# Optimization experiments

Hardware: AMD Instinct MI355X
Metric: run time of the kernel (lower is better)

The kernel has to match this reference:

```python
import jax, jax.numpy as jnp
import numpy as np

NEG_SLOPE = 0.2


def setup_inputs() -> dict:
    key = jax.random.key(0)
    k1, k2, k3, k4, k5 = jax.random.split(key, 5)
    N, E = 50000, 800000
    IN, H, O = 128, 4, 32
    x = jax.random.normal(k1, (N, IN), dtype=jnp.float32)
    edge_index = jax.random.randint(k2, (2, E), 0, N, dtype=jnp.int64)
    weight = jax.random.normal(k3, (IN, H, O), dtype=jnp.float32) * 0.05
    att_weight = jax.random.normal(k4, (H, 2 * O), dtype=jnp.float32) * 0.05
    bias = jax.random.normal(k5, (H * O,), dtype=jnp.float32) * 0.05
    return {"x": x, "edge_index": edge_index, "weight": weight,
            "att_weight": att_weight, "bias": bias}


def reference(x, edge_index, weight, att_weight, bias):
    # GAT forward, eval mode (dropout=0), concat=True.
    N = x.shape[0]
    H, O = weight.shape[1], weight.shape[2]
    # Linear transform: [N, H, O]
    h = jnp.einsum('ni,iho->nho', x, weight)
    src, dst = edge_index[0], edge_index[1]  # message src -> dst
    h_i = h[dst]   # target features per edge  [E, H, O]
    h_j = h[src]   # source features per edge  [E, H, O]
    # Attention logits: leaky_relu(att . [h_i || h_j])  -> [E, H]
    a_i, a_j = att_weight[:, :O], att_weight[:, O:]
    alpha = jnp.einsum('eho,ho->eh', h_i, a_i) + jnp.einsum('eho,ho->eh', h_j, a_j)
    alpha = jax.nn.leaky_relu(alpha, NEG_SLOPE)
    # Segment softmax over incoming edges of each dst node.
    amax = jax.ops.segment_max(alpha, dst, num_segments=N)      # [N, H]
    ex = jnp.exp(alpha - amax[dst])                             # [E, H]
    denom = jax.ops.segment_sum(ex, dst, num_segments=N)        # [N, H]
    coef = ex / (denom[dst] + 1e-16)                            # [E, H]
    # Weighted scatter-aggregate of source messages.
    out = jax.ops.segment_sum(h_j * coef[..., None], dst, num_segments=N)  # [N, H, O]
    out = out.reshape(N, H * O) + bias
    return out
```

## Files before the change

### kernel.cpp

```cpp
#include <hip/hip_runtime.h>
#include <hip/hip_fp16.h>
#include <math.h>

#define NEG_SLOPE 0.2f

typedef __attribute__((ext_vector_type(8))) short bf16x8;
typedef __attribute__((ext_vector_type(4))) short short4v;
typedef __attribute__((ext_vector_type(4))) float f32x4;
typedef __attribute__((ext_vector_type(8))) unsigned short u16x8;

__device__ __forceinline__ float lrelu(float x) { return x > 0.f ? x : NEG_SLOPE * x; }

__device__ __forceinline__ short f2bf(float f) {
    unsigned u = __float_as_uint(f);
    u += 0x7fff + ((u >> 16) & 1);
    return (short)(u >> 16);
}

__global__ __launch_bounds__(256) void k_gemm(const float* __restrict__ x,
                                              const float* __restrict__ w,
                                              const float* __restrict__ att,
                                              __half* __restrict__ hout,
                                              float* __restrict__ adi,
                                              float* __restrict__ adj,
                                              int* __restrict__ gcur, int N) {
    __shared__ short SH[24576];
    const int t = threadIdx.x;
    const int row0 = blockIdx.x * 64;

    if (blockIdx.x == 0) {
        gcur[t] = 0; gcur[t + 256] = 0; gcur[t + 512] = 0; gcur[t + 768] = 0;
    }

    #pragma unroll
    for (int i = 0; i < 8; ++i) {
        int idx = t + 256 * i;
        int r = idx >> 5, c4 = (idx & 31) * 4;
        float4 v = make_float4(0.f, 0.f, 0.f, 0.f);
        if (row0 + r < N) v = *(const float4*)(x + (size_t)(row0 + r) * 128 + c4);
        short4v sv;
        sv.x = f2bf(v.x); sv.y = f2bf(v.y); sv.z = f2bf(v.z); sv.w = f2bf(v.w);
        *(short4v*)&SH[(r * 128 + c4) ^ ((r & 7) << 3)] = sv;
    }
    {
        int c = t & 127, kh = (t >> 7) * 64;
        for (int kb = 0; kb < 16; ++kb) {
            int k = kh + kb * 4;
            short4v sv;
            sv.x = f2bf(w[(size_t)(k + 0) * 128 + c]);
            sv.y = f2bf(w[(size_t)(k + 1) * 128 + c]);
            sv.z = f2bf(w[(size_t)(k + 2) * 128 + c]);
            sv.w = f2bf(w[(size_t)(k + 3) * 128 + c]);
            *(short4v*)&SH[8192 + ((c * 128 + k) ^ ((c & 7) << 3))] = sv;
        }
    }
    __syncthreads();

    const int wv = t >> 6, lane = t & 63;
    const int lr = lane & 15, kg = lane >> 4;

    f32x4 acc[8];
    #pragma unroll
    for (int n = 0; n < 8; ++n) acc[n] = (f32x4){0.f, 0.f, 0.f, 0.f};

    #pragma unroll
    for (int kk = 0; kk < 4; ++kk) {
        const int k0 = kk * 32 + kg * 8;
        int r = wv * 16 + lr;
        bf16x8 a = *(const bf16x8*)&SH[(r * 128 + k0) ^ ((r & 7) << 3)];
        bf16x8 b[8];
        #pragma unroll
        for (int n = 0; n < 8; ++n) {
            int c = n * 16 + lr;
            b[n] = *(const bf16x8*)&SH[8192 + ((c * 128 + k0) ^ ((c & 7) << 3))];
        }
        #pragma unroll
        for (int n = 0; n < 8; ++n)
            acc[n] = __builtin_amdgcn_mfma_f32_16x16x32_bf16(a, b[n], acc[n], 0, 0, 0);
    }

    #pragma unroll
    for (int reg = 0; reg < 4; ++reg) {
        int r = row0 + wv * 16 + kg * 4 + reg;
        if (r < N) {
            __half* hp = hout + (size_t)r * 128 + lr;
            #pragma unroll
            for (int n = 0; n < 8; ++n)
                hp[n * 16] = __float2half(acc[n][reg]);
        }
    }

    __syncthreads();
    float* attF = (float*)&SH[8192];
    attF[t] = att[t];
    #pragma unroll
    for (int reg = 0; reg < 4; ++reg) {
        int row = wv * 16 + kg * 4 + reg;
        #pragma unroll
        for (int n = 0; n < 8; ++n) {
            int col = n * 16 + lr;
            SH[(row * 128 + col) ^ ((row & 7) << 3)] =
                (short)__half_as_ushort(__float2half(acc[n][reg]));
        }
    }
    __syncthreads();
    {
        int row = t >> 2, head = t & 3;
        int grow = row0 + row;
        if (grow < N) {
            float si = 0.f, sj = 0.f;
            #pragma unroll
            for (int j = 0; j < 32; ++j) {
                int jj = (j + row) & 31;
                float hv = __half2float(__ushort_as_half(
                    (unsigned short)SH[(row * 128 + head * 32 + jj) ^ ((row & 7) << 3)]));
                si += hv * attF[head * 64 + jj];
                sj += hv * attF[head * 64 + 32 + jj];
            }
            adi[grow * 4 + head] = si;
            adj[grow * 4 + head] = sj;
        }
    }
}

__global__ __launch_bounds__(512) void k_bin(const int* __restrict__ ei,
                                             int* __restrict__ gcur,
                                             unsigned* __restrict__ bins,
                                             int E, int nbkt, int cap) {
    __shared__ int lcnt[1024];
    __shared__ int lbase[1024];
    const int t = threadIdx.x;
    lcnt[t] = 0; lcnt[t + 512] = 0;
    __syncthreads();

    const int e0 = blockIdx.x * 4096;
    const int ne = min(4096, E - e0);

    int bkt[8], rank[8];
    unsigned pk[8];
    #pragma unroll
    for (int k = 0; k < 8; ++k) {
        int idx = t + k * 512;
        if (idx < ne) {
            int e = e0 + idx;
            int src = ei[e], dst = ei[E + e];
            int b = dst >> 6;
            bkt[k] = b;
            pk[k] = ((unsigned)(dst & 63) << 24) | (unsigned)src;
            rank[k] = atomicAdd(&lcnt[b], 1);
        } else bkt[k] = -1;
    }
    __syncthreads();
    for (int j = t; j < nbkt; j += 512)
        if (lcnt[j] > 0) lbase[j] = atomicAdd(&gcur[j], lcnt[j]);
    __syncthreads();
    #pragma unroll
    for (int k = 0; k < 8; ++k) {
        if (bkt[k] >= 0)
            bins[(size_t)bkt[k] * cap + lbase[bkt[k]] + rank[k]] = pk[k];
    }
}

#define CSR_MAX 1536

__global__ __launch_bounds__(512) void k_bucket_node(
        const unsigned* __restrict__ bins,
        const int* __restrict__ gcur,
        const __half* __restrict__ h,
        const float* __restrict__ adi,
        const float* __restrict__ adjf,
        const float* __restrict__ bias,
        float* __restrict__ out, int N, int cap) {
    __shared__ int csrL[CSR_MAX];
    __shared__ int cnt[64];
    __shared__ int beg[64];
    __shared__ int cur[64];
    const int b = blockIdx.x, t = threadIdx.x;
    const int sz = min(gcur[b], CSR_MAX);
    const unsigned* myb = bins + (size_t)b * cap;

    if (t < 64) cnt[t] = 0;
    __syncthreads();
    for (int i = t; i < sz; i += 512) atomicAdd(&cnt[myb[i] >> 24], 1);
    __syncthreads();
    if (t < 64) {
        int v = cnt[t];
        int s = v;
        #pragma unroll
        for (int off = 1; off < 64; off <<= 1) {
            int u = __shfl_up(s, off);
            if (t >= off) s += u;
        }
        beg[t] = s - v;
        cur[t] = s - v;
    }
    __syncthreads();
    for (int i = t; i < sz; i += 512) {
        unsigned p = myb[i];
        int pos = atomicAdd(&cur[p >> 24], 1);
        csrL[pos] = (int)(p & 0xFFFFFFu);
    }
    __syncthreads();

    const int wv = t >> 6, lane = t & 63;
    const int q = lane >> 4, s = lane & 15;
    const int head = s >> 2;

    for (int n = wv; n < 64; n += 8) {
        int node = b * 64 + n;
        if (node >= N) break;
        const int bg = beg[n];
        const int deg = cnt[n];
        const float ai = adi[node * 4 + head];

        float acc[8] = {0.f, 0.f, 0.f, 0.f, 0.f, 0.f, 0.f, 0.f};
        float dsum = 0.f;

        for (int i = 0; i < deg; i += 16) {
            int idx[4];
            float aj[4];
            u16x8 hv[4];
            #pragma unroll
            for (int bb = 0; bb < 4; ++bb) {
                int ee = i + 4 * bb + q;
                idx[bb] = csrL[bg + (ee < deg ? ee : 0)];
            }
            #pragma unroll
            for (int bb = 0; bb < 4; ++bb) {
                aj[bb] = adjf[idx[bb] * 4 + head];
                hv[bb] = *(const u16x8*)(h + (size_t)idx[bb] * 128 + s * 8);
            }
            #pragma unroll
            for (int bb = 0; bb < 4; ++bb) {
                int ee = i + 4 * bb + q;
                float ex = (ee < deg) ? __expf(lrelu(ai + aj[bb])) : 0.f;
                dsum += ex;
                #pragma unroll
                for (int k = 0; k < 8; ++k)
                    acc[k] += __half2float(__ushort_as_half(hv[bb][k])) * ex;
            }
        }

        #pragma unroll
        for (int k = 0; k < 8; ++k) {
            acc[k] += __shfl_xor(acc[k], 16);
            acc[k] += __shfl_xor(acc[k], 32);
        }
        dsum += __shfl_xor(dsum, 16);
        dsum += __shfl_xor(dsum, 32);

        if (q == 0) {
            float inv = 1.f / (dsum + 1e-16f);
            const float4* b4 = (const float4*)(bias + s * 8);
            float4 bv0 = b4[0], bv1 = b4[1];
            float4 o0 = make_float4(acc[0] * inv + bv0.x, acc[1] * inv + bv0.y,
                                    acc[2] * inv + bv0.z, acc[3] * inv + bv0.w);
            float4 o1 = make_float4(acc[4] * inv + bv1.x, acc[5] * inv + bv1.y,
                                    acc[6] * inv + bv1.z, acc[7] * inv + bv1.w);
            float4* op = (float4*)(out + (size_t)node * 128 + s * 8);
            op[0] = o0;
            op[1] = o1;
        }
    }
}

extern "C" void kernel_launch(void* const* d_in, const int* in_sizes, int n_in,
                              void* d_out, int out_size, void* d_ws, size_t ws_size,
                              hipStream_t stream) {
    const float* x    = (const float*)d_in[0];
    const int*   ei   = (const int*)d_in[1];
    const float* w    = (const float*)d_in[2];
    const float* att  = (const float*)d_in[3];
    const float* bias = (const float*)d_in[4];

    const int N = in_sizes[0] / 128;
    const int E = in_sizes[1] / 2;

    const int NBKT = (N + 63) >> 6;
    const int CAP  = 1536;

    float* out = (float*)d_out;
    char*  wsb = (char*)d_ws;

    __half* h   = (__half*)wsb;
    float*  adi = (float*)(wsb + (size_t)N * 128 * 2);
    float*  adj = adi + (size_t)N * 4;
    int* gcur   = (int*)(adj + (size_t)N * 4);
    unsigned* bins = (unsigned*)(gcur + 1024);

    k_gemm<<<(N + 63) / 64, 256, 0, stream>>>(x, w, att, h, adi, adj, gcur, N);
    k_bin<<<(E + 4095) / 4096, 512, 0, stream>>>(ei, gcur, bins, E, NBKT, CAP);
    k_bucket_node<<<NBKT, 512, 0, stream>>>(bins, gcur, (const __half*)h,
                                            adi, adj, bias, out, N, CAP);
}
```

Baseline: 76.67 us.

## Split bucket CSR build from node aggregation into separate kernels

The fused bucket-and-aggregate kernel is split in two. The first kernel builds a per-bucket CSR in global memory along with per-node begin and degree arrays. The second launches one wavefront per node to do the softmax-weighted gather. This is meant to give better load balance and more parallelism than 782 blocks of 512 threads each looping over 64 nodes. The cost is an extra kernel launch and a global write and read of the CSR.

```diff
diff --git a/kernel.cpp b/kernel.cpp
--- a/kernel.cpp
+++ b/kernel.cpp
@@ -161,27 +161,23 @@
     }
 }
 
-#define CSR_MAX 1536
-
-__global__ __launch_bounds__(512) void k_bucket_node(
-        const unsigned* __restrict__ bins,
-        const int* __restrict__ gcur,
-        const __half* __restrict__ h,
-        const float* __restrict__ adi,
-        const float* __restrict__ adjf,
-        const float* __restrict__ bias,
-        float* __restrict__ out, int N, int cap) {
-    __shared__ int csrL[CSR_MAX];
+__global__ __launch_bounds__(256) void k_bucket(const unsigned* __restrict__ bins,
+                                                const int* __restrict__ gcur,
+                                                int* __restrict__ begG,
+                                                int* __restrict__ degG,
+                                                int* __restrict__ csr,
+                                                int N, int cap) {
     __shared__ int cnt[64];
     __shared__ int beg[64];
     __shared__ int cur[64];
     const int b = blockIdx.x, t = threadIdx.x;
-    const int sz = min(gcur[b], CSR_MAX);
+    const int sz = min(gcur[b], cap);
     const unsigned* myb = bins + (size_t)b * cap;
+    int* mycsr = csr + (size_t)b * cap;
 
     if (t < 64) cnt[t] = 0;
     __syncthreads();
-    for (int i = t; i < sz; i += 512) atomicAdd(&cnt[myb[i] >> 24], 1);
+    for (int i = t; i < sz; i += 256) atomicAdd(&cnt[myb[i] >> 24], 1);
     __syncthreads();
     if (t < 64) {
         int v = cnt[t];
@@ -193,74 +189,82 @@
         }
         beg[t] = s - v;
         cur[t] = s - v;
-    }
-    __syncthreads();
-    for (int i = t; i < sz; i += 512) {
+        int node = b * 64 + t;
+        if (node < N) { begG[node] = b * cap + (s - v); degG[node] = v; }
+    }
+    __syncthreads();
+    for (int i = t; i < sz; i += 256) {
         unsigned p = myb[i];
         int pos = atomicAdd(&cur[p >> 24], 1);
-        csrL[pos] = (int)(p & 0xFFFFFFu);
-    }
-    __syncthreads();
-
-    const int wv = t >> 6, lane = t & 63;
+        mycsr[pos] = (int)(p & 0xFFFFFFu);
+    }
+}
+
+__global__ __launch_bounds__(256) void k_node(const int* __restrict__ begG,
+                                              const int* __restrict__ degG,
+                                              const int* __restrict__ csr,
+                                              const __half* __restrict__ h,
+                                              const float* __restrict__ adi,
+                                              const float* __restrict__ adjf,
+                                              const float* __restrict__ bias,
+                                              float* __restrict__ out, int N) {
+    int node = (blockIdx.x * blockDim.x + threadIdx.x) >> 6;
+    if (node >= N) return;
+    const int lane = threadIdx.x & 63;
     const int q = lane >> 4, s = lane & 15;
     const int head = s >> 2;
 
-    for (int n = wv; n < 64; n += 8) {
-        int node = b * 64 + n;
-        if (node >= N) break;
-        const int bg = beg[n];
-        const int deg = cnt[n];
-        const float ai = adi[node * 4 + head];
-
-        float acc[8] = {0.f, 0.f, 0.f, 0.f, 0.f, 0.f, 0.f, 0.f};
-        float dsum = 0.f;
-
-        for (int i = 0; i < deg; i += 16) {
-            int idx[4];
-            float aj[4];
-            u16x8 hv[4];
+    const int beg = begG[node];
+    const int deg = degG[node];
+    const float ai = adi[node * 4 + head];
+
+    float acc[8] = {0.f, 0.f, 0.f, 0.f, 0.f, 0.f, 0.f, 0.f};
+    float dsum = 0.f;
+
+    for (int i = 0; i < deg; i += 16) {
+        int idx[4];
+        float aj[4];
+        u16x8 hv[4];
+        #pragma unroll
+        for (int bb = 0; bb < 4; ++bb) {
+            int ee = i + 4 * bb + q;
+            idx[bb] = csr[beg + (ee < deg ? ee : 0)];
+        }
+        #pragma unroll
+        for (int bb = 0; bb < 4; ++bb) {
+            aj[bb] = adjf[idx[bb] * 4 + head];
+            hv[bb] = *(const u16x8*)(h + (size_t)idx[bb] * 128 + s * 8);
+        }
+        #pragma unroll
+        for (int bb = 0; bb < 4; ++bb) {
+            int ee = i + 4 * bb + q;
+            float ex = (ee < deg) ? __expf(lrelu(ai + aj[bb])) : 0.f;
+            dsum += ex;
             #pragma unroll
-            for (int bb = 0; bb < 4; ++bb) {
-                int ee = i + 4 * bb + q;
-                idx[bb] = csrL[bg + (ee < deg ? ee : 0)];
-            }
-            #pragma unroll
-            for (int bb = 0; bb < 4; ++bb) {
-                aj[bb] = adjf[idx[bb] * 4 + head];
-                hv[bb] = *(const u16x8*)(h + (size_t)idx[bb] * 128 + s * 8);
-            }
-            #pragma unroll
-            for (int bb = 0; bb < 4; ++bb) {
-                int ee = i + 4 * bb + q;
-                float ex = (ee < deg) ? __expf(lrelu(ai + aj[bb])) : 0.f;
-                dsum += ex;
-                #pragma unroll
-                for (int k = 0; k < 8; ++k)
-                    acc[k] += __half2float(__ushort_as_half(hv[bb][k])) * ex;
-            }
-        }
-
-        #pragma unroll
-        for (int k = 0; k < 8; ++k) {
-            acc[k] += __shfl_xor(acc[k], 16);
-            acc[k] += __shfl_xor(acc[k], 32);
-        }
-        dsum += __shfl_xor(dsum, 16);
-        dsum += __shfl_xor(dsum, 32);
-
-        if (q == 0) {
-            float inv = 1.f / (dsum + 1e-16f);
-            const float4* b4 = (const float4*)(bias + s * 8);
-            float4 bv0 = b4[0], bv1 = b4[1];
-            float4 o0 = make_float4(acc[0] * inv + bv0.x, acc[1] * inv + bv0.y,
-                                    acc[2] * inv + bv0.z, acc[3] * inv + bv0.w);
-            float4 o1 = make_float4(acc[4] * inv + bv1.x, acc[5] * inv + bv1.y,
-                                    acc[6] * inv + bv1.z, acc[7] * inv + bv1.w);
-            float4* op = (float4*)(out + (size_t)node * 128 + s * 8);
-            op[0] = o0;
-            op[1] = o1;
-        }
+            for (int k = 0; k < 8; ++k)
+                acc[k] += __half2float(__ushort_as_half(hv[bb][k])) * ex;
+        }
+    }
+
+    #pragma unroll
+    for (int k = 0; k < 8; ++k) {
+        acc[k] += __shfl_xor(acc[k], 16);
+        acc[k] += __shfl_xor(acc[k], 32);
+    }
+    dsum += __shfl_xor(dsum, 16);
+    dsum += __shfl_xor(dsum, 32);
+
+    if (q == 0) {
+        float inv = 1.f / (dsum + 1e-16f);
+        const float4* b4 = (const float4*)(bias + s * 8);
+        float4 bv0 = b4[0], bv1 = b4[1];
+        float4 o0 = make_float4(acc[0] * inv + bv0.x, acc[1] * inv + bv0.y,
+                                acc[2] * inv + bv0.z, acc[3] * inv + bv0.w);
+        float4 o1 = make_float4(acc[4] * inv + bv1.x, acc[5] * inv + bv1.y,
+                                acc[6] * inv + bv1.z, acc[7] * inv + bv1.w);
+        float4* op = (float4*)(out + (size_t)node * 128 + s * 8);
+        op[0] = o0;
+        op[1] = o1;
     }
 }
 
@@ -286,10 +290,19 @@
     float*  adi = (float*)(wsb + (size_t)N * 128 * 2);
     float*  adj = adi + (size_t)N * 4;
     int* gcur   = (int*)(adj + (size_t)N * 4);
-    unsigned* bins = (unsigned*)(gcur + 1024);
+    int* begG   = gcur + 1024;
+    int* degG   = begG + N;
+    int* csr    = degG + N;
+    unsigned* bins = (unsigned*)(csr + (size_t)NBKT * CAP);
 
     k_gemm<<<(N + 63) / 64, 256, 0, stream>>>(x, w, att, h, adi, adj, gcur, N);
     k_bin<<<(E + 4095) / 4096, 512, 0, stream>>>(ei, gcur, bins, E, NBKT, CAP);
-    k_bucket_node<<<NBKT, 512, 0, stream>>>(bins, gcur, (const __half*)h,
-                                            adi, adj, bias, out, N, CAP);
-}
+    k_bucket<<<NBKT, 256, 0, stream>>>(bins, gcur, begG, degG, csr, N, CAP);
+
+    {
+        long long total = (long long)N * 64;
+        int blocks = (int)((total + 255) / 256);
+        k_node<<<blocks, 256, 0, stream>>>(begG, degG, csr, (const __half*)h,
+                                           adi, adj, bias, out, N);
+    }
+}
```

Measured after the change: 76.25 us. No clear change (-0.6%).
